# Performance work log

Hardware: AMD Instinct MI355X
Metric: run time of the kernel (lower is better)

The kernel has to match this reference:

```python
import jax, jax.numpy as jnp
import numpy as np

C = 0.01          # curvature
EPS = 1e-6        # eps used in midpoint / weight normalization (matches torch code)
MIN_NORM = 1e-10  # numerical floor for norms
BALL_EPS = 1e-5   # projection margin


def _norm(x):
    return jnp.sqrt(jnp.clip(jnp.sum(x * x, axis=-1, keepdims=True), MIN_NORM))


def log_map_zero(x, c):
    sc = jnp.sqrt(c)
    n = _norm(x)
    return jnp.arctanh(jnp.clip(sc * n, -1.0 + BALL_EPS, 1.0 - BALL_EPS)) * x / (sc * n)


def exp_map_zero(v, c):
    sc = jnp.sqrt(c)
    n = _norm(v)
    return jnp.tanh(sc * n) * v / (sc * n)


def project_to_ball(x, c):
    n = _norm(x)
    maxn = (1.0 - BALL_EPS) / jnp.sqrt(c)
    return jnp.where(n > maxn, x * (maxn / n), x)


def mobius_add(x, y, c):
    x2 = jnp.sum(x * x, axis=-1, keepdims=True)
    y2 = jnp.sum(y * y, axis=-1, keepdims=True)
    xy = jnp.sum(x * y, axis=-1, keepdims=True)
    num = (1.0 + 2.0 * c * xy + c * y2) * x + (1.0 - c * x2) * y
    den = 1.0 + 2.0 * c * xy + (c * c) * x2 * y2
    return num / jnp.clip(den, MIN_NORM)


def setup_inputs() -> dict:
    N, E, R, D = 50000, 400000, 230, 16
    key = jax.random.key(0)
    ks = jax.random.split(key, 8)
    h_hyper = project_to_ball(0.1 * jax.random.normal(ks[0], (N, D), dtype=jnp.float32), C)
    node_norm = jax.random.uniform(ks[1], (N, 1), dtype=jnp.float32)
    xav = float(np.sqrt(2.0 / (D + D)))
    rel_weight = xav * jax.random.normal(ks[2], (R, D, D), dtype=jnp.float32)
    loop_weight = xav * jax.random.normal(ks[3], (D, D), dtype=jnp.float32)
    rel_emb = 0.1 * jax.random.normal(ks[4], (R, D), dtype=jnp.float32)
    src = jax.random.randint(ks[5], (E,), 0, N, dtype=jnp.int32)
    dst = jax.random.randint(ks[6], (E,), 0, N, dtype=jnp.int32)
    etype = jax.random.randint(ks[7], (E,), 0, R, dtype=jnp.int32)
    return {"h_hyper": h_hyper, "node_norm": node_norm, "rel_weight": rel_weight,
            "loop_weight": loop_weight, "rel_emb": rel_emb,
            "src": src, "dst": dst, "etype": etype}


def reference(h_hyper, node_norm, rel_weight, loop_weight, rel_emb, src, dst, etype):
    c = C
    N = h_hyper.shape[0]
    # --- msg_func: Mobius matvec per edge (log -> gathered GEMM -> +rel -> exp) ---
    h_tan = log_map_zero(h_hyper, c)                                  # [N, D]
    msg_tan = jnp.einsum('ei,eio->eo', h_tan[src], rel_weight[etype])  # [E, D]
    msg_tan = msg_tan + rel_emb[etype]
    msg = exp_map_zero(msg_tan, c)                                    # [E, D]
    # --- reduce_func: Einstein midpoint per destination node ---
    en = node_norm[dst, 0]                                            # [E] per-edge dst norm
    norm_sum = jax.ops.segment_sum(en, dst, num_segments=N)           # [N]
    w = en / (norm_sum[dst] + EPS)                                    # normalized weights
    lam = 2.0 / (1.0 - c * jnp.sum(msg * msg, axis=-1) + EPS)         # Lorentz factors [E]
    wl = w * lam
    numer = jax.ops.segment_sum(wl[:, None] * msg, dst, num_segments=N)  # [N, D]
    denom = jax.ops.segment_sum(wl, dst, num_segments=N) + EPS           # [N]
    h_agg = project_to_ball(numer / denom[:, None], c)
    # --- self loop in tangent space, combined with Mobius addition ---
    loop_hyp = exp_map_zero(h_tan @ loop_weight, c)
    h_new = mobius_add(h_agg, loop_hyp, c)
    return h_new
```

## Files before the change

kernel.cpp:

```cpp
#include <hip/hip_runtime.h>

#define C_CURV   0.01f
#define SQRT_C   0.1f
#define EPS_W    1e-6f
#define MIN_NORM 1e-10f
#define BALL_EPS 1e-5f
#define CAP      32
#define WSTRIDE  130

typedef __attribute__((ext_vector_type(4))) float f32x4;

__device__ __forceinline__ float fast_rcp(float x)   { return __builtin_amdgcn_rcpf(x); }
__device__ __forceinline__ float fast_sqrt(float x)  { return __builtin_amdgcn_sqrtf(x); }
__device__ __forceinline__ float fast_rsqrt(float x) { return __builtin_amdgcn_rsqf(x); }
__device__ __forceinline__ float tanh_over_x(float x) {
    float t = __expf(2.0f * x);
    return (t - 1.0f) * fast_rcp((t + 1.0f) * x);
}
__device__ __forceinline__ unsigned bf16_rne(float x) {
    unsigned u = __float_as_uint(x);
    return (u + 0x7FFFu + ((u >> 16) & 1u)) >> 16;
}
__device__ __forceinline__ float group4_sum(float v) {
    v += __shfl_xor(v, 1, 64);
    v += __shfl_xor(v, 2, 64);
    return v;
}

__global__ __launch_bounds__(256) void fhnn_zero(int* __restrict__ cursor, int n4) {
    int i = blockIdx.x * blockDim.x + threadIdx.x;
    if (i < n4) ((int4*)cursor)[i] = make_int4(0, 0, 0, 0);
}

__global__ __launch_bounds__(256) void fhnn_prepscatter(
        const float* __restrict__ h_hyper,
        const float* __restrict__ loop_weight,
        const int*   __restrict__ src,
        const int*   __restrict__ dst,
        const int*   __restrict__ etype,
        float* __restrict__ h_tan,
        float* __restrict__ loop_hyp,
        float* __restrict__ ynorm,
        int*      __restrict__ cursor,
        unsigned* __restrict__ bucket,
        int N, int E, int blocksN) {
    if ((int)blockIdx.x >= blocksN) {
        int e = (blockIdx.x - blocksN) * blockDim.x + threadIdx.x;
        if (e >= E) return;
        int t = dst[e];
        int slot = atomicAdd(&cursor[t], 1);
        if (slot < CAP)
            bucket[(size_t)t * CAP + slot] = (unsigned)src[e] | ((unsigned)etype[e] << 16);
        return;
    }
    __shared__ float Wl[256];
    Wl[threadIdx.x] = loop_weight[threadIdx.x];
    __syncthreads();

    int gid = blockIdx.x * blockDim.x + threadIdx.x;
    int t = gid >> 2, j = gid & 3;
    if (t >= N) return;

    f32x4 x = ((const f32x4*)h_hyper)[gid];

    float sq  = group4_sum(x.x * x.x + x.y * x.y + x.z * x.z + x.w * x.w);
    float n   = fast_sqrt(fmaxf(sq, MIN_NORM));
    float scn = SQRT_C * n;
    float z   = fminf(scn, 1.0f - BALL_EPS);
    float at  = 0.5f * __logf((1.0f + z) * fast_rcp(1.0f - z));
    float s   = at * fast_rcp(scn);
    f32x4 ht  = x * s;
    ((f32x4*)h_tan)[gid] = ht;

    f32x4 acc = (f32x4)(0.0f);
    #pragma unroll
    for (int q = 0; q < 4; ++q) {
        float h0 = __shfl(ht.x, q, 4);
        float h1 = __shfl(ht.y, q, 4);
        float h2 = __shfl(ht.z, q, 4);
        float h3 = __shfl(ht.w, q, 4);
        const f32x4* Wrow = (const f32x4*)Wl;
        acc += h0 * Wrow[(4 * q + 0) * 4 + j];
        acc += h1 * Wrow[(4 * q + 1) * 4 + j];
        acc += h2 * Wrow[(4 * q + 2) * 4 + j];
        acc += h3 * Wrow[(4 * q + 3) * 4 + j];
    }
    float sq2 = group4_sum(acc.x * acc.x + acc.y * acc.y + acc.z * acc.z + acc.w * acc.w);
    float n2  = fast_sqrt(fmaxf(sq2, MIN_NORM));
    float f2  = tanh_over_x(SQRT_C * n2);
    ((f32x4*)loop_hyp)[gid] = acc * f2;
    if (j == 0) ynorm[t] = sq2 * f2 * f2;
}

#define WSTEP(HS, I, WSP) { \
    uint2 w = *(const uint2*)((WSP) + 8 * (I)); \
    f32x4 wvv; \
    wvv.x = __uint_as_float(w.x << 16); \
    wvv.y = __uint_as_float(w.x & 0xFFFF0000u); \
    wvv.z = __uint_as_float(w.y << 16); \
    wvv.w = __uint_as_float(w.y & 0xFFFF0000u); \
    a4 += (HS) * wvv; }

#define EDGE(H0, H1, H2, H3, RR, VALID) { \
    const unsigned* Ws = lds_w + (unsigned)(RR) * WSTRIDE + 2u * (unsigned)j; \
    f32x4 a4 = (f32x4)(0.0f); \
    WSTEP((H0).x,  0, Ws) WSTEP((H0).y,  1, Ws) WSTEP((H0).z,  2, Ws) WSTEP((H0).w,  3, Ws) \
    WSTEP((H1).x,  4, Ws) WSTEP((H1).y,  5, Ws) WSTEP((H1).z,  6, Ws) WSTEP((H1).w,  7, Ws) \
    WSTEP((H2).x,  8, Ws) WSTEP((H2).y,  9, Ws) WSTEP((H2).z, 10, Ws) WSTEP((H2).w, 11, Ws) \
    WSTEP((H3).x, 12, Ws) WSTEP((H3).y, 13, Ws) WSTEP((H3).z, 14, Ws) WSTEP((H3).w, 15, Ws) \
    f32x4 v = a4 + *(const f32x4*)(relE + (RR) * 16 + 4 * j); \
    float sq = group4_sum(v.x * v.x + v.y * v.y + v.z * v.z + v.w * v.w); \
    float f  = tanh_over_x(SQRT_C * fast_sqrt(fmaxf(sq, MIN_NORM))); \
    float m2 = f * f * sq; \
    float lam = 2.0f * fast_rcp(1.0f - C_CURV * m2 + EPS_W); \
    float cf = (VALID) ? (f * lam) : 0.0f; \
    accM += v * cf; \
    accL += (VALID) ? lam : 0.0f; }

#define EDGEBLK(PK, KIDX) { \
    bool vld = (KIDX) < cn; \
    int s = vld ? (int)((PK) & 0xFFFFu) : 0; \
    int r = vld ? (int)((PK) >> 16) : 0; \
    const f32x4* H = (const f32x4*)(h_tan + (size_t)s * 16); \
    f32x4 q0 = H[0], q1 = H[1], q2 = H[2], q3 = H[3]; \
    EDGE(q0, q1, q2, q3, r, vld) }

__global__ __launch_bounds__(1024, 1) void fhnn_reduce(
        const float*    __restrict__ h_tan,
        const float*    __restrict__ rel_weight,
        const float*    __restrict__ rel_emb,
        const unsigned* __restrict__ bucket,
        const int*      __restrict__ cursor,
        const float*    __restrict__ node_norm,
        const float*    __restrict__ loop_hyp,
        const float*    __restrict__ ynorm,
        float*          __restrict__ out,
        int N, int R) {
    extern __shared__ unsigned lds_w[];
    const int relOff = ((R * WSTRIDE + 3) & ~3);
    float* relE = (float*)(lds_w + relOff);

    for (int idx = threadIdx.x; idx < R * 64; idx += blockDim.x) {
        int r = idx >> 6, c4 = idx & 63;
        f32x4 w = ((const f32x4*)rel_weight)[idx];
        lds_w[r * WSTRIDE + 2 * c4]     = bf16_rne(w.x) | (bf16_rne(w.y) << 16);
        lds_w[r * WSTRIDE + 2 * c4 + 1] = bf16_rne(w.z) | (bf16_rne(w.w) << 16);
    }
    for (int idx = threadIdx.x; idx < R * 16; idx += blockDim.x)
        relE[idx] = rel_emb[idx];
    __syncthreads();

    int wv   = threadIdx.x >> 6;
    int lane = threadIdx.x & 63;
    int grp  = lane >> 4;
    int slot = (lane >> 2) & 3;
    int j    = lane & 3;
    int wstart  = (blockIdx.x * 16 + wv) * 4 + grp;
    int nstride = gridDim.x * 16 * 4;

    int cnF = 0;
    unsigned pk0 = 0u;
    if (wstart < N) {
        cnF = cursor[wstart];
        pk0 = bucket[(size_t)wstart * CAP + slot];
    }

    for (int t = wstart; t < N; t += nstride) {
        int tn = t + nstride;
        int cnF_n = 0;
        unsigned pk0_n = 0u;
        if (tn < N) {
            cnF_n = cursor[tn];
            pk0_n = bucket[(size_t)tn * CAP + slot];
        }

        int cnFull = cnF;
        int cn = min(cnFull, CAP);
        size_t bbase = (size_t)t * CAP + slot;

        unsigned pk1 = bucket[bbase + 4];
        unsigned pk2 = bucket[bbase + 8];
        unsigned pk3 = bucket[bbase + 12];

        float en = node_norm[t];
        f32x4 y  = ((const f32x4*)(loop_hyp + (size_t)t * 16))[j];
        float y2 = ynorm[t];

        f32x4 accM = (f32x4)(0.0f);
        float accL = 0.0f;

        EDGEBLK(pk0, slot)
        if (__any(cn >  4)) EDGEBLK(pk1, slot + 4)
        if (__any(cn >  8)) EDGEBLK(pk2, slot + 8)
        if (__any(cn > 12)) EDGEBLK(pk3, slot + 12)
        if (__any(cn > 16)) {
            for (int k = 16 + slot; k < cn; k += 4) {
                unsigned pk = bucket[(size_t)t * CAP + k];
                int s = (int)(pk & 0xFFFFu);
                int r = (int)(pk >> 16);
                const f32x4* H = (const f32x4*)(h_tan + (size_t)s * 16);
                f32x4 q0 = H[0], q1 = H[1], q2 = H[2], q3 = H[3];
                EDGE(q0, q1, q2, q3, r, true)
            }
        }

        #pragma unroll
        for (int m = 4; m <= 8; m <<= 1) {
            accM.x += __shfl_xor(accM.x, m, 64);
            accM.y += __shfl_xor(accM.y, m, 64);
            accM.z += __shfl_xor(accM.z, m, 64);
            accM.w += __shfl_xor(accM.w, m, 64);
            accL   += __shfl_xor(accL,   m, 64);
        }

        float wsc   = en * fast_rcp((float)cnFull * en + EPS_W);
        float denom = wsc * accL + EPS_W;
        float rs    = wsc * fast_rcp(denom);
        f32x4 x     = accM * rs;

        float x2 = group4_sum(x.x * x.x + x.y * x.y + x.z * x.z + x.w * x.w);
        const float maxn  = (1.0f - BALL_EPS) / SQRT_C;
        const float maxn2 = maxn * maxn;
        bool over = (x2 > maxn2);
        float scale = over ? (maxn * fast_rsqrt(x2)) : 1.0f;
        x *= scale;
        float x2p = over ? maxn2 : x2;

        float xy = group4_sum(x.x * y.x + x.y * y.y + x.z * y.z + x.w * y.w);

        float a1  = 1.0f + 2.0f * C_CURV * xy + C_CURV * y2;
        float b1  = 1.0f - C_CURV * x2p;
        f32x4 num = a1 * x + b1 * y;
        float d2  = 1.0f + 2.0f * C_CURV * xy + C_CURV * C_CURV * x2p * y2;
        if (slot == 0)
            ((f32x4*)out)[t * 4 + j] = num * fast_rcp(fmaxf(d2, MIN_NORM));

        cnF = cnF_n;
        pk0 = pk0_n;
    }
}

extern "C" void kernel_launch(void* const* d_in, const int* in_sizes, int n_in,
                              void* d_out, int out_size, void* d_ws, size_t ws_size,
                              hipStream_t stream) {
    const float* h_hyper     = (const float*)d_in[0];
    const float* node_norm   = (const float*)d_in[1];
    const float* rel_weight  = (const float*)d_in[2];
    const float* loop_weight = (const float*)d_in[3];
    const float* rel_emb     = (const float*)d_in[4];
    const int*   src         = (const int*)d_in[5];
    const int*   dst         = (const int*)d_in[6];
    const int*   etype       = (const int*)d_in[7];

    const int N = in_sizes[1];
    const int E = in_sizes[5];
    const int R = in_sizes[2] / 256;

    char* ws = (char*)d_ws;
    size_t offs = 0;
    auto alloc = [&](size_t bytes) -> void* {
        void* p = ws + offs;
        offs += (bytes + 255) & ~(size_t)255;
        return p;
    };
    float*    h_tan    = (float*)alloc((size_t)N * 16 * 4);
    float*    loop_hyp = (float*)alloc((size_t)N * 16 * 4);
    float*    ynorm    = (float*)alloc((size_t)N * 4);
    unsigned* bucket   = (unsigned*)alloc((size_t)N * CAP * 4);
    int*      cursor   = (int*)alloc((size_t)N * 4);
    int nZero4 = (N + 3) >> 2;

    int relOff   = ((R * WSTRIDE + 3) & ~3);
    int ldsBytes = (relOff + R * 16) * 4;
    hipFuncSetAttribute((const void*)fhnn_reduce,
                        hipFuncAttributeMaxDynamicSharedMemorySize, ldsBytes);

    const int threads = 256;
    int blocksZ  = (nZero4 + threads - 1) / threads;
    int blocksN4 = (N * 4 + threads - 1) / threads;
    int blocksE1 = (E + threads - 1) / threads;

    fhnn_zero<<<blocksZ, threads, 0, stream>>>(cursor, nZero4);
    fhnn_prepscatter<<<blocksN4 + blocksE1, threads, 0, stream>>>(
        h_hyper, loop_weight, src, dst, etype, h_tan, loop_hyp, ynorm, cursor, bucket,
        N, E, blocksN4);
    fhnn_reduce<<<256, 1024, ldsBytes, stream>>>(
        h_tan, rel_weight, rel_emb, bucket, cursor, node_norm, loop_hyp, ynorm,
        (float*)d_out, N, R);
}
```

Measured before the change: 62.82 us.

## Prepack bf16 relation weights globally and read them from cache instead of LDS

The bf16 packing of relation weights moves into the zeroing kernel, which writes a packed global buffer. The reduce kernel no longer stages weights and embeddings into shared memory per block. It reads them straight from global memory (L1/L2 cached, about 118KB) and launches 2048 blocks of 256 threads instead of 256 blocks of 1024 with a large LDS footprint. This removes the per-block LDS fill and barrier and frees occupancy, but the per-edge weight reads now go through the vector memory cache path rather than LDS, which may be slower.

After: 67.96 us. 8.2% more time.

```diff
diff --git a/kernel.cpp b/kernel.cpp
--- a/kernel.cpp
+++ b/kernel.cpp
@@ -6,7 +6,6 @@
 #define MIN_NORM 1e-10f
 #define BALL_EPS 1e-5f
 #define CAP      32
-#define WSTRIDE  130
 
 typedef __attribute__((ext_vector_type(4))) float f32x4;
 
@@ -27,9 +26,21 @@
     return v;
 }
 
-__global__ __launch_bounds__(256) void fhnn_zero(int* __restrict__ cursor, int n4) {
+__global__ __launch_bounds__(256) void fhnn_zero_pack(
+        int* __restrict__ cursor, int n4,
+        const float* __restrict__ rel_weight,
+        unsigned* __restrict__ wpack,
+        int nPack) {
     int i = blockIdx.x * blockDim.x + threadIdx.x;
     if (i < n4) ((int4*)cursor)[i] = make_int4(0, 0, 0, 0);
+    int p = i - n4;
+    if (p >= 0 && p < nPack) {
+        f32x4 w = ((const f32x4*)rel_weight)[p];
+        uint2 o;
+        o.x = bf16_rne(w.x) | (bf16_rne(w.y) << 16);
+        o.y = bf16_rne(w.z) | (bf16_rne(w.w) << 16);
+        ((uint2*)wpack)[p] = o;
+    }
 }
 
 __global__ __launch_bounds__(256) void fhnn_prepscatter(
@@ -93,7 +104,7 @@
 }
 
 #define WSTEP(HS, I, WSP) { \
-    uint2 w = *(const uint2*)((WSP) + 8 * (I)); \
+    uint2 w = *((WSP) + (I)); \
     f32x4 wvv; \
     wvv.x = __uint_as_float(w.x << 16); \
     wvv.y = __uint_as_float(w.x & 0xFFFF0000u); \
@@ -102,13 +113,13 @@
     a4 += (HS) * wvv; }
 
 #define EDGE(H0, H1, H2, H3, RR, VALID) { \
-    const unsigned* Ws = lds_w + (unsigned)(RR) * WSTRIDE + 2u * (unsigned)j; \
+    const uint2* Ws = (const uint2*)(wpack + (size_t)(RR) * 128) + (unsigned)j; \
     f32x4 a4 = (f32x4)(0.0f); \
-    WSTEP((H0).x,  0, Ws) WSTEP((H0).y,  1, Ws) WSTEP((H0).z,  2, Ws) WSTEP((H0).w,  3, Ws) \
-    WSTEP((H1).x,  4, Ws) WSTEP((H1).y,  5, Ws) WSTEP((H1).z,  6, Ws) WSTEP((H1).w,  7, Ws) \
-    WSTEP((H2).x,  8, Ws) WSTEP((H2).y,  9, Ws) WSTEP((H2).z, 10, Ws) WSTEP((H2).w, 11, Ws) \
-    WSTEP((H3).x, 12, Ws) WSTEP((H3).y, 13, Ws) WSTEP((H3).z, 14, Ws) WSTEP((H3).w, 15, Ws) \
-    f32x4 v = a4 + *(const f32x4*)(relE + (RR) * 16 + 4 * j); \
+    WSTEP((H0).x,  0, Ws) WSTEP((H0).y,  4, Ws) WSTEP((H0).z,  8, Ws) WSTEP((H0).w, 12, Ws) \
+    WSTEP((H1).x, 16, Ws) WSTEP((H1).y, 20, Ws) WSTEP((H1).z, 24, Ws) WSTEP((H1).w, 28, Ws) \
+    WSTEP((H2).x, 32, Ws) WSTEP((H2).y, 36, Ws) WSTEP((H2).z, 40, Ws) WSTEP((H2).w, 44, Ws) \
+    WSTEP((H3).x, 48, Ws) WSTEP((H3).y, 52, Ws) WSTEP((H3).z, 56, Ws) WSTEP((H3).w, 60, Ws) \
+    f32x4 v = a4 + *(const f32x4*)(rel_emb + (size_t)(RR) * 16 + 4 * j); \
     float sq = group4_sum(v.x * v.x + v.y * v.y + v.z * v.z + v.w * v.w); \
     float f  = tanh_over_x(SQRT_C * fast_sqrt(fmaxf(sq, MIN_NORM))); \
     float m2 = f * f * sq; \
@@ -125,9 +136,9 @@
     f32x4 q0 = H[0], q1 = H[1], q2 = H[2], q3 = H[3]; \
     EDGE(q0, q1, q2, q3, r, vld) }
 
-__global__ __launch_bounds__(1024, 1) void fhnn_reduce(
+__global__ __launch_bounds__(256) void fhnn_reduce(
         const float*    __restrict__ h_tan,
-        const float*    __restrict__ rel_weight,
+        const unsigned* __restrict__ wpack,
         const float*    __restrict__ rel_emb,
         const unsigned* __restrict__ bucket,
         const int*      __restrict__ cursor,
@@ -135,28 +146,14 @@
         const float*    __restrict__ loop_hyp,
         const float*    __restrict__ ynorm,
         float*          __restrict__ out,
-        int N, int R) {
-    extern __shared__ unsigned lds_w[];
-    const int relOff = ((R * WSTRIDE + 3) & ~3);
-    float* relE = (float*)(lds_w + relOff);
-
-    for (int idx = threadIdx.x; idx < R * 64; idx += blockDim.x) {
-        int r = idx >> 6, c4 = idx & 63;
-        f32x4 w = ((const f32x4*)rel_weight)[idx];
-        lds_w[r * WSTRIDE + 2 * c4]     = bf16_rne(w.x) | (bf16_rne(w.y) << 16);
-        lds_w[r * WSTRIDE + 2 * c4 + 1] = bf16_rne(w.z) | (bf16_rne(w.w) << 16);
-    }
-    for (int idx = threadIdx.x; idx < R * 16; idx += blockDim.x)
-        relE[idx] = rel_emb[idx];
-    __syncthreads();
-
-    int wv   = threadIdx.x >> 6;
+        int N) {
+    int wid  = (blockIdx.x * blockDim.x + threadIdx.x) >> 6;
     int lane = threadIdx.x & 63;
     int grp  = lane >> 4;
     int slot = (lane >> 2) & 3;
     int j    = lane & 3;
-    int wstart  = (blockIdx.x * 16 + wv) * 4 + grp;
-    int nstride = gridDim.x * 16 * 4;
+    int wstart  = wid * 4 + grp;
+    int nstride = (gridDim.x * blockDim.x >> 6) * 4;
 
     int cnF = 0;
     unsigned pk0 = 0u;
@@ -268,23 +265,21 @@
     float*    ynorm    = (float*)alloc((size_t)N * 4);
     unsigned* bucket   = (unsigned*)alloc((size_t)N * CAP * 4);
     int*      cursor   = (int*)alloc((size_t)N * 4);
+    unsigned* wpack    = (unsigned*)alloc((size_t)R * 128 * 4);
     int nZero4 = (N + 3) >> 2;
-
-    int relOff   = ((R * WSTRIDE + 3) & ~3);
-    int ldsBytes = (relOff + R * 16) * 4;
-    hipFuncSetAttribute((const void*)fhnn_reduce,
-                        hipFuncAttributeMaxDynamicSharedMemorySize, ldsBytes);
+    int nPack  = R * 64;
 
     const int threads = 256;
-    int blocksZ  = (nZero4 + threads - 1) / threads;
+    int blocksZP = (nZero4 + nPack + threads - 1) / threads;
     int blocksN4 = (N * 4 + threads - 1) / threads;
     int blocksE1 = (E + threads - 1) / threads;
-
-    fhnn_zero<<<blocksZ, threads, 0, stream>>>(cursor, nZero4);
+    int blocksR  = 2048;
+
+    fhnn_zero_pack<<<blocksZP, threads, 0, stream>>>(cursor, nZero4, rel_weight, wpack, nPack);
     fhnn_prepscatter<<<blocksN4 + blocksE1, threads, 0, stream>>>(
         h_hyper, loop_weight, src, dst, etype, h_tan, loop_hyp, ynorm, cursor, bucket,
         N, E, blocksN4);
-    fhnn_reduce<<<256, 1024, ldsBytes, stream>>>(
-        h_tan, rel_weight, rel_emb, bucket, cursor, node_norm, loop_hyp, ynorm,
-        (float*)d_out, N, R);
-}
+    fhnn_reduce<<<blocksR, threads, 0, stream>>>(
+        h_tan, wpack, rel_emb, bucket, cursor, node_norm, loop_hyp, ynorm,
+        (float*)d_out, N);
+}
```
